# Kernel optimization log

Measured on AMD Instinct MI355X. Metric: run time of the kernel, lower is better.

The kernel has to match this reference:

```python
import jax, jax.numpy as jnp
import numpy as np

EPS = 1e-5

def _conv1x1(x, w):
    # w: [out_ch, in_ch], x: [n, c, h, w] -> [n, out_ch, h, w]
    return jnp.einsum('oc,nchw->nohw', w, x)

def _bn_relu(x, g, b, m, v):
    # inference-mode BatchNorm2d followed by ReLU
    s = g * jax.lax.rsqrt(v + EPS)
    return jax.nn.relu(x * s[None, :, None, None] + (b - m * s)[None, :, None, None])

def setup_inputs() -> dict:
    N, C, H, W, Kc, K = 8, 512, 128, 128, 512, 19
    keys = iter(jax.random.split(jax.random.key(0), 64))
    d = {}
    d['x'] = jax.random.normal(next(keys), (N, C, H, W), jnp.float32)
    d['proxy'] = jax.random.normal(next(keys), (N, C, K, 1), jnp.float32)
    for nm, shp in [('wp1', (Kc, C)), ('wp2', (Kc, Kc)), ('wo1', (Kc, C)),
                    ('wo2', (Kc, Kc)), ('wd', (Kc, C)), ('wu', (C, Kc))]:
        d[nm] = jax.random.normal(next(keys), shp, jnp.float32) * np.float32(1.0 / np.sqrt(shp[1]))
    for tag, ch in [('p1', Kc), ('p2', Kc), ('o1', Kc), ('o2', Kc), ('d', Kc), ('u', C)]:
        d['g' + tag] = 1.0 + 0.1 * jax.random.normal(next(keys), (ch,), jnp.float32)
        d['b' + tag] = 0.1 * jax.random.normal(next(keys), (ch,), jnp.float32)
        d['m' + tag] = 0.1 * jax.random.normal(next(keys), (ch,), jnp.float32)
        d['v' + tag] = jax.random.uniform(next(keys), (ch,), jnp.float32, 0.5, 1.5)
    return d

def reference(x, proxy,
              wp1, gp1, bp1, mp1, vp1, wp2, gp2, bp2, mp2, vp2,
              wo1, go1, bo1, mo1, vo1, wo2, go2, bo2, mo2, vo2,
              wd, gd, bd, md, vd, wu, gu, bu, mu, vu):
    # scale == 1: no pooling / upsampling
    # f_pixel: two 1x1 conv + BN + ReLU on pixel features
    q = _bn_relu(_conv1x1(x, wp1), gp1, bp1, mp1, vp1)
    q = _bn_relu(_conv1x1(q, wp2), gp2, bp2, mp2, vp2)        # [n, kc, h, w]
    n, kc, h, w = q.shape
    q = q.reshape(n, kc, h * w)                               # [n, kc, hw]
    # f_object on proxy (object region representations)
    k = _bn_relu(_conv1x1(proxy, wo1), go1, bo1, mo1, vo1)
    k = _bn_relu(_conv1x1(k, wo2), go2, bo2, mo2, vo2).reshape(n, kc, -1)  # [n, kc, K]
    # f_down (value)
    v = _bn_relu(_conv1x1(proxy, wd), gd, bd, md, vd).reshape(n, kc, -1)   # [n, kc, K]
    # cross-attention: pixels attend over object regions
    sim = jnp.einsum('ncq,nck->nqk', q, k) * (kc ** -0.5)     # [n, hw, K]
    attn = jax.nn.softmax(sim, axis=-1)
    ctx = jnp.einsum('nqk,nck->ncq', attn, v).reshape(n, kc, h, w)
    # f_up: 1x1 conv + BN + ReLU back to in_channels
    return _bn_relu(_conv1x1(ctx, wu), gu, bu, mu, vu)
```

## Files before the change

kernel.cpp:

```cpp
#include <hip/hip_runtime.h>
#include <stdint.h>

#define HW 16384
#define CH 512
#define KR 19

typedef float f32x4 __attribute__((ext_vector_type(4)));
typedef _Float16 half8 __attribute__((ext_vector_type(8)));
typedef unsigned short us8 __attribute__((ext_vector_type(8)));
typedef unsigned short us4 __attribute__((ext_vector_type(4)));

__device__ __forceinline__ unsigned short f2h(float f) {
    union { _Float16 h; unsigned short u; } v; v.h = (_Float16)f; return v.u;
}
__device__ __forceinline__ float h2f(unsigned short u) {
    union { unsigned short u; _Float16 h; } v; v.u = u; return (float)v.h;
}

__device__ __forceinline__ void gll16(const void* g, void* l) {
    __builtin_amdgcn_global_load_lds(
        (const __attribute__((address_space(1))) unsigned int*)g,
        (__attribute__((address_space(3))) unsigned int*)l,
        16, 0, 0);
}

__global__ void ObjectAttentionBlock_1176821039805_kernel() {}

__global__ __launch_bounds__(256) void prep_kernel(
    const float* __restrict__ wp1, const float* __restrict__ wp2, const float* __restrict__ wu,
    unsigned short* __restrict__ wp1h, unsigned short* __restrict__ wp2h, unsigned short* __restrict__ wuh,
    const float* gp1, const float* bp1, const float* mp1, const float* vp1,
    const float* gp2, const float* bp2, const float* mp2, const float* vp2,
    const float* gu,  const float* bu,  const float* mu,  const float* vu,
    float* __restrict__ cons)
{
    int i = blockIdx.x * 256 + threadIdx.x;
    if (i < CH * CH) {
        wp1h[i] = f2h(wp1[i]);
        wp2h[i] = f2h(wp2[i]);
        wuh[i]  = f2h(wu[i]);
    }
    if (i < CH) {
        float s1 = gp1[i] * rsqrtf(vp1[i] + 1e-5f);
        cons[i] = s1;          cons[512 + i]  = bp1[i] - mp1[i] * s1;
        float s2 = gp2[i] * rsqrtf(vp2[i] + 1e-5f);
        cons[1024 + i] = s2;   cons[1536 + i] = bp2[i] - mp2[i] * s2;
        float su = gu[i] * rsqrtf(vu[i] + 1e-5f);
        cons[2048 + i] = su;   cons[2560 + i] = bu[i] - mu[i] * su;
    }
}

__global__ __launch_bounds__(256) void transpose_kernel(
    const float* __restrict__ x, unsigned short* __restrict__ xT)
{
    __shared__ unsigned short t[64][66];
    const int n  = blockIdx.z;
    const int c0 = blockIdx.y * 64;
    const int m0 = blockIdx.x * 64;
    const int tx = threadIdx.x & 63;
    const int ty = threadIdx.x >> 6;
    const float* xb = x + ((size_t)n * CH + c0) * HW + m0;
    #pragma unroll
    for (int r = 0; r < 16; ++r) {
        int cl = ty * 16 + r;
        t[cl][tx] = f2h(xb[(size_t)cl * HW + tx]);
    }
    __syncthreads();
    unsigned short* xo = xT + ((size_t)n * HW + m0) * CH + c0;
    #pragma unroll
    for (int r = 0; r < 16; ++r) {
        int ml = ty * 16 + r;
        xo[(size_t)ml * CH + tx] = t[tx][ml];
    }
}

__global__ __launch_bounds__(256) void kv1_kernel(
    const float* __restrict__ proxy, const float* __restrict__ wo1, const float* __restrict__ wd,
    const float* go1, const float* bo1, const float* mo1, const float* vo1,
    const float* gd,  const float* bd,  const float* md,  const float* vd,
    float* __restrict__ t1, float* __restrict__ vout)
{
    const int n  = blockIdx.x;
    const int o0 = blockIdx.y * 64;
    const float* px = proxy + (size_t)n * CH * KR;
    for (int idx = threadIdx.x; idx < 64 * KR; idx += 256) {
        int o = o0 + idx / KR;
        int j = idx % KR;
        float a1 = 0.f, a2 = 0.f;
        for (int c = 0; c < CH; ++c) {
            float p = px[c * KR + j];
            a1 += wo1[o * CH + c] * p;
            a2 += wd [o * CH + c] * p;
        }
        float s1 = go1[o] * rsqrtf(vo1[o] + 1e-5f);
        float s2 = gd[o]  * rsqrtf(vd[o]  + 1e-5f);
        t1  [((size_t)n * CH + o) * KR + j] = fmaxf(a1 * s1 + (bo1[o] - mo1[o] * s1), 0.f);
        vout[((size_t)n * CH + o) * KR + j] = fmaxf(a2 * s2 + (bd[o]  - md[o]  * s2), 0.f);
    }
}

__global__ __launch_bounds__(256) void kv2_kernel(
    const float* __restrict__ t1, const float* __restrict__ wo2,
    const float* go2, const float* bo2, const float* mo2, const float* vo2,
    float* __restrict__ kout)
{
    const int n  = blockIdx.x;
    const int o0 = blockIdx.y * 64;
    const float* tb = t1 + (size_t)n * CH * KR;
    for (int idx = threadIdx.x; idx < 64 * KR; idx += 256) {
        int o = o0 + idx / KR;
        int j = idx % KR;
        float a = 0.f;
        for (int c = 0; c < CH; ++c) a += wo2[o * CH + c] * tb[c * KR + j];
        float s = go2[o] * rsqrtf(vo2[o] + 1e-5f);
        kout[((size_t)n * CH + o) * KR + j] = fmaxf(a * s + (bo2[o] - mo2[o] * s), 0.f);
    }
}

__global__ __launch_bounds__(256) void pad_kernel(
    const float* __restrict__ kbuf, const float* __restrict__ vbuf,
    unsigned short* __restrict__ kt, unsigned short* __restrict__ vt)
{
    int idx = blockIdx.x * 256 + threadIdx.x;
    int n = idx >> 16, rem = idx & 65535;
    int j = rem >> 9, c = rem & 511;
    kt[idx] = (j < KR) ? f2h(kbuf[((size_t)(n * CH + c)) * KR + j]) : (unsigned short)0;
    int c2 = rem >> 7, j2 = rem & 127;
    vt[idx] = (j2 < KR) ? f2h(vbuf[((size_t)(n * CH + c2)) * KR + j2]) : (unsigned short)0;
}

template<int MODE, int BN>
__global__ __launch_bounds__(256) void gemm_nt(
    const unsigned short* __restrict__ A,
    const unsigned short* __restrict__ W,
    const float* __restrict__ sc, const float* __restrict__ sh,
    void* __restrict__ outp)
{
    __shared__ __align__(16) char lds_raw[65536];
    float (*epi)[132] = (float (*)[132])lds_raw;

    const int tid  = threadIdx.x;
    const int lane = tid & 63;
    const int wave = tid >> 6;
    const int wm = (tid >> 7) & 1;
    const int wn = (tid >> 6) & 1;
    const int id  = blockIdx.x;
    const int swz = (id & 7) * 512 + (id >> 3);
    const int i0 = (swz >> 2) << 7;
    const int j0 = (swz & 3) << 7;

    const int lrow = lane >> 3;
    const int lsw  = ((lane & 7) ^ (lane >> 3)) * 16;

    f32x4 acc[4][4];
    #pragma unroll
    for (int i = 0; i < 4; ++i)
        #pragma unroll
        for (int j = 0; j < 4; ++j) acc[i][j] = (f32x4){0.f, 0.f, 0.f, 0.f};

    const int arow = wm * 64 + (lane & 15);
    const int brow = wn * 64 + (lane & 15);
    const int kch  = lane >> 4;

    auto stageF = [&](int t) {
        char* db = lds_raw + (t & 1) * 32768;
        #pragma unroll
        for (int q = 0; q < 4; ++q) {
            int rg = wave * 32 + q * 8;
            gll16((const char*)A + ((size_t)(i0 + rg + lrow) * 512 + t * 64) * 2 + lsw,
                  db + rg * 128);
            gll16((const char*)W + ((size_t)(j0 + rg + lrow) * 512 + t * 64) * 2 + lsw,
                  db + 16384 + rg * 128);
        }
    };

    stageF(0);
    __syncthreads();

    for (int t = 0; t < 8; ++t) {
        if (t < 7) stageF(t + 1);
        const unsigned short* stage = (const unsigned short*)(lds_raw + (t & 1) * 32768);
        #pragma unroll
        for (int s = 0; s < 2; ++s) {
            half8 af[4], bw[4];
            #pragma unroll
            for (int u = 0; u < 4; ++u) {
                int ra = arow + u * 16;
                af[u] = *(const half8*)(stage + ra * 64 + (((s * 4 + kch) ^ (ra & 7)) << 3));
                int rb = brow + u * 16;
                bw[u] = *(const half8*)(stage + 8192 + rb * 64 + (((s * 4 + kch) ^ (rb & 7)) << 3));
            }
            #pragma unroll
            for (int i = 0; i < 4; ++i)
                #pragma unroll
                for (int j = 0; j < 4; ++j)
                    acc[i][j] = __builtin_amdgcn_mfma_f32_16x16x32_f16(af[i], bw[j], acc[i][j], 0, 0, 0);
        }
        __syncthreads();
    }

    float scv[4], shv[4];
    #pragma unroll
    for (int j = 0; j < 4; ++j) {
        int gj = j0 + wn * 64 + j * 16 + (lane & 15);
        scv[j] = BN ? sc[gj] : 1.0f;
        shv[j] = BN ? sh[gj] : 0.0f;
    }

    if (MODE == 0) {
        unsigned short* op = (unsigned short*)outp;
        #pragma unroll
        for (int i = 0; i < 4; ++i) {
            int gi = i0 + wm * 64 + i * 16 + (lane >> 4) * 4;
            #pragma unroll
            for (int j = 0; j < 4; ++j) {
                int gj = j0 + wn * 64 + j * 16 + (lane & 15);
                #pragma unroll
                for (int r = 0; r < 4; ++r) {
                    float vv = acc[i][j][r];
                    if (BN) vv = fmaxf(vv * scv[j] + shv[j], 0.f);
                    op[(size_t)(gi + r) * 512 + gj] = f2h(vv);
                }
            }
        }
    } else {
        float* op = (float*)outp;
        const int n  = i0 >> 14;
        const int mb = i0 & (HW - 1);
        #pragma unroll
        for (int h = 0; h < 2; ++h) {
            __syncthreads();
            if (wn == h) {
                #pragma unroll
                for (int j = 0; j < 4; ++j) {
                    int ljh = j * 16 + (lane & 15);
                    #pragma unroll
                    for (int i = 0; i < 4; ++i) {
                        int li = wm * 64 + i * 16 + (lane >> 4) * 4;
                        f32x4 vv;
                        #pragma unroll
                        for (int r = 0; r < 4; ++r)
                            vv[r] = fmaxf(acc[i][j][r] * scv[j] + shv[j], 0.f);
                        *(f32x4*)&epi[ljh][li] = vv;
                    }
                }
            }
            __syncthreads();
            #pragma unroll
            for (int q = 0; q < 8; ++q) {
                int idx = q * 256 + tid;
                int ch = idx >> 5, chunk = idx & 31;
                f32x4 v = *(const f32x4*)&epi[ch][chunk * 4];
                size_t base = ((size_t)(n * 512 + j0 + h * 64 + ch) << 14) + mb + chunk * 4;
                op[base] = v[0]; op[base + 1] = v[1]; op[base + 2] = v[2]; op[base + 3] = v[3];
            }
        }
    }
}

__global__ __launch_bounds__(256) void attn_fused(
    const unsigned short* __restrict__ q2,
    const unsigned short* __restrict__ ktg,
    const unsigned short* __restrict__ vtg,
    unsigned short* __restrict__ ctx)
{
    __shared__ __align__(16) char lds[47104];
    unsigned short* stage = (unsigned short*)lds;
    unsigned short* vt_l  = (unsigned short*)lds;
    unsigned short* att_l = (unsigned short*)(lds + 36864);

    const int tid  = threadIdx.x;
    const int lane = tid & 63;
    const int w    = tid >> 6;
    const int i0   = blockIdx.x * 128;
    const int n    = blockIdx.x >> 7;
    const unsigned short* KT = ktg + n * 65536;
    const unsigned short* VT = vtg + n * 65536;

    size_t gA[4]; int loA[4];
    #pragma unroll
    for (int q = 0; q < 4; ++q) {
        int ca = q * 256 + tid;
        int r = ca >> 3, p = ca & 7;
        gA[q] = (size_t)(i0 + r) * 512 + p * 8;
        loA[q] = r * 64 + ((p ^ (r & 7)) << 3);
    }
    const int rB = tid >> 3, pB = tid & 7;
    const size_t gB = (size_t)rB * 512 + pB * 8;
    const int loB = 8192 + rB * 64 + ((pB ^ (rB & 7)) << 3);

    us8 va[4], vbk;
    #pragma unroll
    for (int q = 0; q < 4; ++q) va[q] = *(const us8*)(q2 + gA[q]);
    vbk = *(const us8*)(KT + gB);

    f32x4 acc[2][2];
    #pragma unroll
    for (int i = 0; i < 2; ++i)
        #pragma unroll
        for (int j = 0; j < 2; ++j) acc[i][j] = (f32x4){0.f, 0.f, 0.f, 0.f};

    const int kch = lane >> 4;
    for (int kk = 0; kk < 8; ++kk) {
        __syncthreads();
        #pragma unroll
        for (int q = 0; q < 4; ++q) *(us8*)(stage + loA[q]) = va[q];
        *(us8*)(stage + loB) = vbk;
        __syncthreads();
        if (kk < 7) {
            #pragma unroll
            for (int q = 0; q < 4; ++q) va[q] = *(const us8*)(q2 + gA[q] + (kk + 1) * 64);
            vbk = *(const us8*)(KT + gB + (kk + 1) * 64);
        }
        #pragma unroll
        for (int s = 0; s < 2; ++s) {
            half8 af[2], bf[2];
            #pragma unroll
            for (int i = 0; i < 2; ++i) {
                int ra = w * 32 + i * 16 + (lane & 15);
                af[i] = *(const half8*)(stage + ra * 64 + (((s * 4 + kch) ^ (ra & 7)) << 3));
            }
            #pragma unroll
            for (int t = 0; t < 2; ++t) {
                int rb = t * 16 + (lane & 15);
                bf[t] = *(const half8*)(stage + 8192 + rb * 64 + (((s * 4 + kch) ^ (rb & 7)) << 3));
            }
            #pragma unroll
            for (int i = 0; i < 2; ++i)
                #pragma unroll
                for (int j = 0; j < 2; ++j)
                    acc[i][j] = __builtin_amdgcn_mfma_f32_16x16x32_f16(af[i], bf[j], acc[i][j], 0, 0, 0);
        }
    }

    const float scale = 0.044194173824159216f;
    const bool v1 = (lane & 15) < 3;
    unsigned short a16[2][4][2];
    #pragma unroll
    for (int i = 0; i < 2; ++i) {
        #pragma unroll
        for (int r = 0; r < 4; ++r) {
            float s0 = acc[i][0][r] * scale;
            float s1v = acc[i][1][r] * scale;
            float m = v1 ? fmaxf(s0, s1v) : s0;
            m = fmaxf(m, __shfl_xor(m, 1));
            m = fmaxf(m, __shfl_xor(m, 2));
            m = fmaxf(m, __shfl_xor(m, 4));
            m = fmaxf(m, __shfl_xor(m, 8));
            float a0 = __expf(s0 - m);
            float a1 = v1 ? __expf(s1v - m) : 0.f;
            float sm = a0 + a1;
            sm += __shfl_xor(sm, 1);
            sm += __shfl_xor(sm, 2);
            sm += __shfl_xor(sm, 4);
            sm += __shfl_xor(sm, 8);
            float inv = 1.0f / sm;
            a16[i][r][0] = f2h(a0 * inv);
            a16[i][r][1] = f2h(a1 * inv);
        }
    }
    #pragma unroll
    for (int i = 0; i < 2; ++i)
        #pragma unroll
        for (int r = 0; r < 4; ++r) {
            int R = w * 32 + i * 16 + (lane >> 4) * 4 + r;
            att_l[R * 40 + (lane & 15)]      = a16[i][r][0];
            att_l[R * 40 + 16 + (lane & 15)] = a16[i][r][1];
        }
    __syncthreads();

    #pragma unroll
    for (int q = 0; q < 8; ++q) {
        int id = q * 256 + tid;
        int c = id >> 2, part = id & 3;
        us8 v = *(const us8*)(VT + (size_t)c * 128 + part * 8);
        *(us4*)(vt_l + c * 36 + part * 8)     = (us4){v[0], v[1], v[2], v[3]};
        *(us4*)(vt_l + c * 36 + part * 8 + 4) = (us4){v[4], v[5], v[6], v[7]};
    }
    __syncthreads();

    half8 a2[2];
    #pragma unroll
    for (int i = 0; i < 2; ++i) {
        int R = w * 32 + i * 16 + (lane & 15);
        a2[i] = *(const half8*)(att_l + R * 40 + (lane >> 4) * 8);
    }
    #pragma unroll
    for (int jc = 0; jc < 4; ++jc) {
        half8 bf[8];
        #pragma unroll
        for (int t = 0; t < 8; ++t) {
            int c = jc * 128 + t * 16 + (lane & 15);
            const unsigned short* pb = vt_l + c * 36 + (lane >> 4) * 8;
            us4 lo = *(const us4*)(pb);
            us4 hi = *(const us4*)(pb + 4);
            us8 u = {lo[0], lo[1], lo[2], lo[3], hi[0], hi[1], hi[2], hi[3]};
            bf[t] = *(half8*)&u;
        }
        #pragma unroll
        for (int i = 0; i < 2; ++i) {
            #pragma unroll
            for (int t = 0; t < 8; ++t) {
                f32x4 o = __builtin_amdgcn_mfma_f32_16x16x32_f16(
                    a2[i], bf[t], (f32x4){0.f, 0.f, 0.f, 0.f}, 0, 0, 0);
                int col = jc * 128 + t * 16 + (lane & 15);
                int row = i0 + w * 32 + i * 16 + (lane >> 4) * 4;
                #pragma unroll
                for (int r = 0; r < 4; ++r)
                    ctx[(size_t)(row + r) * 512 + col] = f2h(o[r]);
            }
        }
    }
}

extern "C" void kernel_launch(void* const* d_in, const int* in_sizes, int n_in,
                              void* d_out, int out_size, void* d_ws, size_t ws_size,
                              hipStream_t stream)
{
    const float* x     = (const float*)d_in[0];
    const float* proxy = (const float*)d_in[1];
    const float* wp1   = (const float*)d_in[2];
    const float* wp2   = (const float*)d_in[3];
    const float* wo1   = (const float*)d_in[4];
    const float* wo2   = (const float*)d_in[5];
    const float* wd    = (const float*)d_in[6];
    const float* wu    = (const float*)d_in[7];
    const float* gp1 = (const float*)d_in[8],  *bp1 = (const float*)d_in[9];
    const float* mp1 = (const float*)d_in[10], *vp1 = (const float*)d_in[11];
    const float* gp2 = (const float*)d_in[12], *bp2 = (const float*)d_in[13];
    const float* mp2 = (const float*)d_in[14], *vp2 = (const float*)d_in[15];
    const float* go1 = (const float*)d_in[16], *bo1 = (const float*)d_in[17];
    const float* mo1 = (const float*)d_in[18], *vo1 = (const float*)d_in[19];
    const float* go2 = (const float*)d_in[20], *bo2 = (const float*)d_in[21];
    const float* mo2 = (const float*)d_in[22], *vo2 = (const float*)d_in[23];
    const float* gd  = (const float*)d_in[24], *bd  = (const float*)d_in[25];
    const float* md  = (const float*)d_in[26], *vd  = (const float*)d_in[27];
    const float* gu  = (const float*)d_in[28], *bu  = (const float*)d_in[29];
    const float* mu  = (const float*)d_in[30], *vu  = (const float*)d_in[31];

    char* ws = (char*)d_ws;
    unsigned short* r0   = (unsigned short*)ws;
    unsigned short* wp1h = (unsigned short*)(ws + 134217728);
    unsigned short* wp2h = wp1h + 262144;
    unsigned short* wuh  = wp2h + 262144;
    float* t1   = (float*)(wuh + 262144);
    float* kbuf = t1 + 8 * CH * KR;
    float* vbuf = kbuf + 8 * CH * KR;
    float* cons = vbuf + 8 * CH * KR;

    float* outf = (float*)d_out;
    unsigned short* outh = (unsigned short*)d_out;
    unsigned short* q1T = outh;
    unsigned short* ktb = outh + 117440512;
    unsigned short* vtb = outh + 117964800;

    prep_kernel<<<1024, 256, 0, stream>>>(wp1, wp2, wu, wp1h, wp2h, wuh,
        gp1, bp1, mp1, vp1, gp2, bp2, mp2, vp2, gu, bu, mu, vu, cons);
    transpose_kernel<<<dim3(256, 8, 8), 256, 0, stream>>>(x, r0);
    kv1_kernel<<<dim3(8, 8), 256, 0, stream>>>(proxy, wo1, wd,
        go1, bo1, mo1, vo1, gd, bd, md, vd, t1, vbuf);
    kv2_kernel<<<dim3(8, 8), 256, 0, stream>>>(t1, wo2, go2, bo2, mo2, vo2, kbuf);
    pad_kernel<<<2048, 256, 0, stream>>>(kbuf, vbuf, ktb, vtb);

    gemm_nt<0, 1><<<4096, 256, 0, stream>>>(r0, wp1h, cons, cons + 512, q1T);
    gemm_nt<0, 1><<<4096, 256, 0, stream>>>(q1T, wp2h, cons + 1024, cons + 1536, r0);
    attn_fused<<<1024, 256, 0, stream>>>(r0, ktb, vtb, r0);
    gemm_nt<1, 1><<<4096, 256, 0, stream>>>(r0, wuh, cons + 2048, cons + 2560, outf);
}
```

Baseline: 725.6 us.

## Halve GEMM k-tile, shrink LDS, prefetch two stages ahead with explicit waitcnt

Restructures the gemm_nt main loop to use 32-wide k-tiles (16 iterations) in a 16KB double buffer with a new row-folded swizzled layout. Loads are issued two tiles ahead and waited on with explicit vmcnt counts and raw barriers instead of __syncthreads, and s_setprio raises priority around the MFMA section. LDS drops from 64KB to about 33KB, so more blocks can be resident per CU. The trade-off is twice as many barriers per tile and a more fragile hand-scheduled wait sequence.

```diff
diff --git a/kernel.cpp b/kernel.cpp
--- a/kernel.cpp
+++ b/kernel.cpp
@@ -136,7 +136,7 @@
     const float* __restrict__ sc, const float* __restrict__ sh,
     void* __restrict__ outp)
 {
-    __shared__ __align__(16) char lds_raw[65536];
+    __shared__ __align__(16) char lds_raw[33792];
     float (*epi)[132] = (float (*)[132])lds_raw;
 
     const int tid  = threadIdx.x;
@@ -149,55 +149,11 @@
     const int i0 = (swz >> 2) << 7;
     const int j0 = (swz & 3) << 7;
 
-    const int lrow = lane >> 3;
-    const int lsw  = ((lane & 7) ^ (lane >> 3)) * 16;
-
-    f32x4 acc[4][4];
-    #pragma unroll
-    for (int i = 0; i < 4; ++i)
-        #pragma unroll
-        for (int j = 0; j < 4; ++j) acc[i][j] = (f32x4){0.f, 0.f, 0.f, 0.f};
-
-    const int arow = wm * 64 + (lane & 15);
-    const int brow = wn * 64 + (lane & 15);
-    const int kch  = lane >> 4;
-
-    auto stageF = [&](int t) {
-        char* db = lds_raw + (t & 1) * 32768;
-        #pragma unroll
-        for (int q = 0; q < 4; ++q) {
-            int rg = wave * 32 + q * 8;
-            gll16((const char*)A + ((size_t)(i0 + rg + lrow) * 512 + t * 64) * 2 + lsw,
-                  db + rg * 128);
-            gll16((const char*)W + ((size_t)(j0 + rg + lrow) * 512 + t * 64) * 2 + lsw,
-                  db + 16384 + rg * 128);
-        }
-    };
-
-    stageF(0);
-    __syncthreads();
-
-    for (int t = 0; t < 8; ++t) {
-        if (t < 7) stageF(t + 1);
-        const unsigned short* stage = (const unsigned short*)(lds_raw + (t & 1) * 32768);
-        #pragma unroll
-        for (int s = 0; s < 2; ++s) {
-            half8 af[4], bw[4];
-            #pragma unroll
-            for (int u = 0; u < 4; ++u) {
-                int ra = arow + u * 16;
-                af[u] = *(const half8*)(stage + ra * 64 + (((s * 4 + kch) ^ (ra & 7)) << 3));
-                int rb = brow + u * 16;
-                bw[u] = *(const half8*)(stage + 8192 + rb * 64 + (((s * 4 + kch) ^ (rb & 7)) << 3));
-            }
-            #pragma unroll
-            for (int i = 0; i < 4; ++i)
-                #pragma unroll
-                for (int j = 0; j < 4; ++j)
-                    acc[i][j] = __builtin_amdgcn_mfma_f32_16x16x32_f16(af[i], bw[j], acc[i][j], 0, 0, 0);
-        }
-        __syncthreads();
-    }
+    const int sl = lane >> 3;
+    const int ss = lane & 7;
+    const int sc_ = ss ^ sl;
+    const int srow = sl + 64 * (sc_ >> 2);
+    const int skof = (sc_ & 3) * 8;
 
     float scv[4], shv[4];
     #pragma unroll
@@ -205,6 +161,60 @@
         int gj = j0 + wn * 64 + j * 16 + (lane & 15);
         scv[j] = BN ? sc[gj] : 1.0f;
         shv[j] = BN ? sh[gj] : 0.0f;
+    }
+    asm volatile("s_waitcnt vmcnt(0)" ::: "memory");
+    __builtin_amdgcn_sched_barrier(0);
+
+    f32x4 acc[4][4];
+    #pragma unroll
+    for (int i = 0; i < 4; ++i)
+        #pragma unroll
+        for (int j = 0; j < 4; ++j) acc[i][j] = (f32x4){0.f, 0.f, 0.f, 0.f};
+
+    const int rl  = lane & 15;
+    const int kch = lane >> 4;
+
+    auto stage = [&](int t) {
+        char* db = lds_raw + (t & 1) * 16384;
+        #pragma unroll
+        for (int q = 0; q < 2; ++q) {
+            int g = q * 4 + wave;
+            gll16((const char*)A + ((size_t)(i0 + g * 8 + srow) * 512 + t * 32 + skof) * 2,
+                  db + g * 1024);
+            gll16((const char*)W + ((size_t)(j0 + g * 8 + srow) * 512 + t * 32 + skof) * 2,
+                  db + 8192 + g * 1024);
+        }
+    };
+
+    stage(0);
+    stage(1);
+
+    for (int t = 0; t < 16; ++t) {
+        if (t < 15) asm volatile("s_waitcnt vmcnt(4)" ::: "memory");
+        else        asm volatile("s_waitcnt vmcnt(0)" ::: "memory");
+        __builtin_amdgcn_sched_barrier(0);
+        __builtin_amdgcn_s_barrier();
+        __builtin_amdgcn_sched_barrier(0);
+
+        const unsigned short* st = (const unsigned short*)(lds_raw + (t & 1) * 16384);
+        __builtin_amdgcn_s_setprio(1);
+        half8 af[4], bw[4];
+        #pragma unroll
+        for (int u = 0; u < 4; ++u) {
+            int la = rl + u * 16;
+            af[u] = *(const half8*)(st + la * 64 + (((wm * 4 + kch) ^ (la & 7)) << 3));
+            bw[u] = *(const half8*)(st + 4096 + la * 64 + (((wn * 4 + kch) ^ (la & 7)) << 3));
+        }
+        #pragma unroll
+        for (int i = 0; i < 4; ++i)
+            #pragma unroll
+            for (int j = 0; j < 4; ++j)
+                acc[i][j] = __builtin_amdgcn_mfma_f32_16x16x32_f16(af[i], bw[j], acc[i][j], 0, 0, 0);
+        __builtin_amdgcn_s_setprio(0);
+        __builtin_amdgcn_sched_barrier(0);
+        __builtin_amdgcn_s_barrier();
+        __builtin_amdgcn_sched_barrier(0);
+        if (t < 14) stage(t + 2);
     }
 
     if (MODE == 0) {
```

Result: no change. 730.5 us (+0.7%).
